# Performance work log

Hardware: AMD Instinct MI355X
Metric: run time of the kernel (lower is better)

Reference implementation:

```python
import jax, jax.numpy as jnp
import numpy as np

N, E, H = 50000, 800000, 64  # nodes, edges, hidden
EPS = 1e-5
SLOPE = 0.2  # LeakyReLU negative slope


def setup_inputs() -> dict:
    key = jax.random.key(0)
    ks = jax.random.split(key, 8)
    return {
        "x": jax.random.normal(ks[0], (N, H), dtype=jnp.float32),
        "edge_weight": jax.random.uniform(ks[1], (E,), dtype=jnp.float32),
        "edge_index": jax.random.randint(ks[2], (2, E), 0, N, dtype=jnp.int64),
        # Linear weights, torch convention [out_features, in_features], bias=False
        "w1": jax.random.normal(ks[3], (H, 2 * H), dtype=jnp.float32) * 0.05,
        "w2": jax.random.normal(ks[4], (H, H), dtype=jnp.float32) * 0.05,
        "w3": jax.random.normal(ks[5], (H, H), dtype=jnp.float32) * 0.05,
        # LayerNorm affine params
        "g1": jnp.ones((2 * H,), jnp.float32), "b1": jnp.zeros((2 * H,), jnp.float32),
        "g2": jnp.ones((H,), jnp.float32), "b2": jnp.zeros((H,), jnp.float32),
        "g3": jnp.ones((H,), jnp.float32), "b3": jnp.zeros((H,), jnp.float32),
    }


def _ln_act_lin(h, g, b, w):
    # LayerNorm -> LeakyReLU(0.2) -> Linear(bias=False), as in MLP(norm='layer')
    mu = jnp.mean(h, axis=-1, keepdims=True)
    var = jnp.mean((h - mu) ** 2, axis=-1, keepdims=True)
    h = (h - mu) * jax.lax.rsqrt(var + EPS) * g + b
    h = jnp.where(h > 0, h, SLOPE * h)
    return h @ w.T


def reference(x, edge_weight, edge_index, w1, w2, w3, g1, b1, g2, b2, g3, b3):
    src, tgt = edge_index[0], edge_index[1]  # x_j = source, x_i = target
    x_j = x[src]                              # [E, H] gather
    x_i = x[tgt]                              # [E, H] gather
    m = jnp.concatenate([x_i, edge_weight[:, None] * (x_j - x_i)], axis=-1)  # [E, 2H]
    m = _ln_act_lin(m, g1, b1, w1)
    m = _ln_act_lin(m, g2, b2, w2)
    m = _ln_act_lin(m, g3, b3, w3)            # [E, H]
    agg = jax.ops.segment_max(m, tgt, num_segments=N)  # EdgeConv aggr='max'
    agg = jnp.where(jnp.isfinite(agg), agg, 0.0)       # isolated nodes -> 0
    return agg + x                             # residual (ResBlock)
```

## Files before the change

### kernel.cpp

```cpp
#include <hip/hip_runtime.h>

#define NN 50000
#define NE 800000
#define NT (NE / 32)

#define CNT_OFF   0u
#define BASE_OFF  204800u
#define PART_OFF  409600u
#define SLOT_OFF  417792u
#define SRCW_OFF  3670016u
#define M_OFF     (1u << 24)
#define WS_NEEDED ((size_t)(1u << 24) + (size_t)NE * 64u * 2u)
#define PB 196

typedef __bf16 bf16x8 __attribute__((ext_vector_type(8)));
typedef float f32x16 __attribute__((ext_vector_type(16)));
typedef unsigned short u16x2 __attribute__((ext_vector_type(2)));

union U4 { unsigned u[4]; __bf16 h[8]; bf16x8 v; };
union PKU { unsigned u; u16x2 v; };

__device__ __forceinline__ unsigned pkpair(float a, float b) {
  union { unsigned u; __bf16 h[2]; } r;
  r.h[0] = (__bf16)a; r.h[1] = (__bf16)b;
  return r.u;
}
__device__ __forceinline__ float bflo(unsigned u) { return __uint_as_float(u << 16); }
__device__ __forceinline__ float bfhi(unsigned u) { return __uint_as_float(u & 0xFFFF0000u); }
__device__ __forceinline__ unsigned pkmaxu16(unsigned a, unsigned b) {
  PKU x, y, r; x.u = a; y.u = b;
  r.v = __builtin_elementwise_max(x.v, y.v);
  return r.u;
}

extern "C" __global__ void __launch_bounds__(256)
scatter_kernel(const int* __restrict__ ei, unsigned* __restrict__ cnt,
               unsigned* __restrict__ slot) {
  const int e = blockIdx.x * 256 + threadIdx.x;
  if (e < NE) {
    int t = ei[NE + e];
    t = min(max(t, 0), NN - 1);
    slot[e] = atomicAdd(cnt + t, 1u);
  }
}

extern "C" __global__ void __launch_bounds__(256)
scan_a_kernel(const unsigned* __restrict__ cnt, unsigned* __restrict__ partial) {
  __shared__ unsigned wsum[4];
  const int t = threadIdx.x, wv = t >> 6, ln = t & 63;
  const int i = blockIdx.x * 256 + t;
  unsigned v = (i < NN) ? cnt[i] : 0u;
  #pragma unroll
  for (int d = 1; d < 64; d <<= 1) v += (unsigned)__shfl_up((int)v, d) * (ln >= d ? 1u : 0u);
  if (ln == 63) wsum[wv] = v;
  __syncthreads();
  if (t == 0) partial[blockIdx.x] = wsum[0] + wsum[1] + wsum[2] + wsum[3];
}

extern "C" __global__ void __launch_bounds__(256)
scan_c_kernel(const unsigned* __restrict__ cnt, const unsigned* __restrict__ partial,
              unsigned* __restrict__ base) {
  __shared__ unsigned pscan[256];
  __shared__ unsigned wsum[4];
  const int t = threadIdx.x, wv = t >> 6, ln = t & 63;
  const unsigned pv = (t < PB) ? partial[t] : 0u;
  unsigned s = pv;
  #pragma unroll
  for (int d = 1; d < 64; d <<= 1) s += (unsigned)__shfl_up((int)s, d) * (ln >= d ? 1u : 0u);
  if (ln == 63) wsum[wv] = s;
  __syncthreads();
  unsigned woff = 0;
  #pragma unroll
  for (int k = 0; k < 4; ++k) woff += (k < wv) ? wsum[k] : 0u;
  pscan[t] = woff + s - pv;
  if (blockIdx.x == 0 && t == 255) base[NN] = woff + s;
  __syncthreads();
  const unsigned blockoff = pscan[blockIdx.x];
  const int i = blockIdx.x * 256 + t;
  const unsigned v = (i < NN) ? cnt[i] : 0u;
  unsigned s2 = v;
  #pragma unroll
  for (int d = 1; d < 64; d <<= 1) s2 += (unsigned)__shfl_up((int)s2, d) * (ln >= d ? 1u : 0u);
  if (ln == 63) wsum[wv] = s2;
  __syncthreads();
  unsigned woff2 = 0;
  #pragma unroll
  for (int k = 0; k < 4; ++k) woff2 += (k < wv) ? wsum[k] : 0u;
  if (i < NN) base[i] = blockoff + woff2 + s2 - v;
}

extern "C" __global__ void __launch_bounds__(256)
reorder_kernel(const int* __restrict__ ei, const float* __restrict__ ew,
               const unsigned* __restrict__ base, const unsigned* __restrict__ slot,
               uint2* __restrict__ srcw) {
  const int e = blockIdx.x * 256 + threadIdx.x;
  if (e < NE) {
    const int s = min(max(ei[e], 0), NN - 1);
    const int t = min(max(ei[NE + e], 0), NN - 1);
    const unsigned pos = base[t] + slot[e];
    uint2 rec;
    rec.x = (unsigned)s | ((unsigned)t << 16);
    rec.y = __float_as_uint(ew[e]);
    srcw[pos] = rec;
  }
}

extern "C" __global__ void __launch_bounds__(256, 3)
edge_mlp_kernel(const float* __restrict__ x, const float* __restrict__ w1,
                const float* __restrict__ w2, const float* __restrict__ w3,
                const float* __restrict__ g1, const float* __restrict__ b1,
                const float* __restrict__ g2, const float* __restrict__ b2,
                const float* __restrict__ g3, const float* __restrict__ b3,
                const uint2* __restrict__ srcw,
                unsigned short* __restrict__ pmax) {
  __shared__ unsigned lds_w[8192];
  const int tid = threadIdx.x;

  #pragma unroll 1
  for (int s = tid; s < 1024; s += 256) {
    const int F = s >> 6, L = s & 63;
    const int t = F >> 1, mt = F & 1;
    const int gg = L >> 5, o = (L & 31) + 32 * mt;
    const float* p = w1 + o * 128 + 16 * t + 8 * gg;
    unsigned* d = &lds_w[(unsigned)(F * 64 + L) * 4u];
    d[0] = pkpair(p[0], p[1]); d[1] = pkpair(p[2], p[3]);
    d[2] = pkpair(p[4], p[5]); d[3] = pkpair(p[6], p[7]);
  }
  #pragma unroll 1
  for (int s = tid; s < 1024; s += 256) {
    const int which = s >> 9, r = s & 511;
    const int F = r >> 6, L = r & 63;
    const int t = F >> 1, mt = F & 1;
    const int gg = L >> 5, o = (L & 31) + 32 * mt;
    const float* W = which ? w3 : w2;
    const float* p = W + o * 64 + 16 * t + 4 * gg;
    unsigned* d = &lds_w[(unsigned)((16 + which * 8 + F) * 64 + L) * 4u];
    d[0] = pkpair(p[0], p[1]); d[1] = pkpair(p[2], p[3]);
    d[2] = pkpair(p[8], p[9]); d[3] = pkpair(p[10], p[11]);
  }
  __syncthreads();

  const int lane = tid & 63;
  const int el = lane & 31;
  const int g = lane >> 5;
  const bf16x8* wfrag = (const bf16x8*)lds_w;

  const int wid = blockIdx.x * 4 + (tid >> 6);
  const int nw = gridDim.x * 4;

  int tile = wid;
  int pvs = 0, pvt = 0; float pw = 0.f;
  if (tile < NT) {
    const uint2 rec = srcw[tile * 32 + el];
    pvs = (int)(rec.x & 0xFFFFu); pvt = (int)(rec.x >> 16); pw = __uint_as_float(rec.y);
  }

  while (tile < NT) {
    asm volatile("" ::: "memory");

    const int p = tile * 32 + el;
    const int vsrc = pvs, vtgt = pvt;
    const float wgt = pw;

    const float* xi = x + (size_t)vtgt * 64 + 8 * g;
    const float* xj = x + (size_t)vsrc * 64 + 8 * g;

    unsigned mp[32];
    float sum = 0.f, ssq = 0.f;
    #pragma unroll
    for (int t = 0; t < 4; ++t) {
      float4 a = *(const float4*)(xi + 16 * t);
      float4 b = *(const float4*)(xi + 16 * t + 4);
      float4 c = *(const float4*)(xj + 16 * t);
      float4 d4 = *(const float4*)(xj + 16 * t + 4);
      float lo[8] = {a.x, a.y, a.z, a.w, b.x, b.y, b.z, b.w};
      float up[8] = {wgt * (c.x - a.x), wgt * (c.y - a.y), wgt * (c.z - a.z), wgt * (c.w - a.w),
                     wgt * (d4.x - b.x), wgt * (d4.y - b.y), wgt * (d4.z - b.z), wgt * (d4.w - b.w)};
      #pragma unroll
      for (int pp = 0; pp < 4; ++pp) {
        mp[4 * t + pp] = pkpair(lo[2 * pp], lo[2 * pp + 1]);
        mp[16 + 4 * t + pp] = pkpair(up[2 * pp], up[2 * pp + 1]);
      }
      #pragma unroll
      for (int j = 0; j < 8; ++j) {
        sum += lo[j] + up[j];
        ssq += lo[j] * lo[j] + up[j] * up[j];
      }
    }

    const int ntile = tile + nw;
    if (ntile < NT) {
      const uint2 rec = srcw[ntile * 32 + el];
      pvs = (int)(rec.x & 0xFFFFu); pvt = (int)(rec.x >> 16); pw = __uint_as_float(rec.y);
    }

    sum += __shfl_xor(sum, 32);
    ssq += __shfl_xor(ssq, 32);
    const float mean1 = sum * (1.f / 128.f);
    const float rstd1 = rsqrtf(ssq * (1.f / 128.f) - mean1 * mean1 + 1e-5f);
    const float c01 = -mean1 * rstd1;

    U4 B1[8];
    #pragma unroll
    for (int t = 0; t < 8; ++t) {
      const int kb = ((t < 4) ? 16 * t : 64 + 16 * (t - 4)) + 8 * g;
      float4 ga = *(const float4*)(g1 + kb);
      float4 gb = *(const float4*)(g1 + kb + 4);
      float4 ba = *(const float4*)(b1 + kb);
      float4 bb = *(const float4*)(b1 + kb + 4);
      float gv[8] = {ga.x, ga.y, ga.z, ga.w, gb.x, gb.y, gb.z, gb.w};
      float bv[8] = {ba.x, ba.y, ba.z, ba.w, bb.x, bb.y, bb.z, bb.w};
      #pragma unroll
      for (int pp = 0; pp < 4; ++pp) {
        const unsigned u = mp[4 * t + pp];
        float v0 = fmaf(bflo(u), rstd1, c01);
        float v1 = fmaf(bfhi(u), rstd1, c01);
        v0 = fmaf(v0, gv[2 * pp], bv[2 * pp]);
        v1 = fmaf(v1, gv[2 * pp + 1], bv[2 * pp + 1]);
        v0 = fmaxf(v0, 0.2f * v0);
        v1 = fmaxf(v1, 0.2f * v1);
        B1[t].h[2 * pp] = (__bf16)v0;
        B1[t].h[2 * pp + 1] = (__bf16)v1;
      }
    }

    f32x16 A0, A1;
    #pragma unroll
    for (int i = 0; i < 16; ++i) { A0[i] = 0.f; A1[i] = 0.f; }
    #pragma unroll
    for (int t = 0; t < 8; ++t) {
      A0 = __builtin_amdgcn_mfma_f32_32x32x16_bf16(wfrag[(2 * t + 0) * 64 + lane], B1[t].v, A0, 0, 0, 0);
      A1 = __builtin_amdgcn_mfma_f32_32x32x16_bf16(wfrag[(2 * t + 1) * 64 + lane], B1[t].v, A1, 0, 0, 0);
    }

    float s2 = 0.f, q2 = 0.f;
    #pragma unroll
    for (int i = 0; i < 16; ++i) {
      s2 += A0[i] + A1[i];
      q2 += A0[i] * A0[i] + A1[i] * A1[i];
    }
    s2 += __shfl_xor(s2, 32); q2 += __shfl_xor(q2, 32);
    const float mean2 = s2 * (1.f / 64.f);
    const float rstd2 = rsqrtf(q2 * (1.f / 64.f) - mean2 * mean2 + 1e-5f);
    const float c02 = -mean2 * rstd2;

    U4 B2[4];
    #pragma unroll
    for (int t2 = 0; t2 < 4; ++t2) {
      const int kb = 16 * t2 + 4 * g;
      float4 gA = *(const float4*)(g2 + kb);
      float4 gB = *(const float4*)(g2 + kb + 8);
      float4 bA = *(const float4*)(b2 + kb);
      float4 bB = *(const float4*)(b2 + kb + 8);
      float gv[8] = {gA.x, gA.y, gA.z, gA.w, gB.x, gB.y, gB.z, gB.w};
      float bv[8] = {bA.x, bA.y, bA.z, bA.w, bB.x, bB.y, bB.z, bB.w};
      #pragma unroll
      for (int j = 0; j < 8; ++j) {
        const int reg = 4 * (2 * (t2 & 1) + (j >> 2)) + (j & 3);
        float v = (t2 >> 1) ? A1[reg] : A0[reg];
        v = fmaf(v, rstd2, c02);
        v = fmaf(v, gv[j], bv[j]);
        v = fmaxf(v, 0.2f * v);
        B2[t2].h[j] = (__bf16)v;
      }
    }

    #pragma unroll
    for (int i = 0; i < 16; ++i) { A0[i] = 0.f; A1[i] = 0.f; }
    #pragma unroll
    for (int t2 = 0; t2 < 4; ++t2) {
      A0 = __builtin_amdgcn_mfma_f32_32x32x16_bf16(wfrag[(16 + 2 * t2 + 0) * 64 + lane], B2[t2].v, A0, 0, 0, 0);
      A1 = __builtin_amdgcn_mfma_f32_32x32x16_bf16(wfrag[(16 + 2 * t2 + 1) * 64 + lane], B2[t2].v, A1, 0, 0, 0);
    }

    float s3 = 0.f, q3 = 0.f;
    #pragma unroll
    for (int i = 0; i < 16; ++i) {
      s3 += A0[i] + A1[i];
      q3 += A0[i] * A0[i] + A1[i] * A1[i];
    }
    s3 += __shfl_xor(s3, 32); q3 += __shfl_xor(q3, 32);
    const float mean3 = s3 * (1.f / 64.f);
    const float rstd3 = rsqrtf(q3 * (1.f / 64.f) - mean3 * mean3 + 1e-5f);
    const float c03 = -mean3 * rstd3;

    U4 B3[4];
    #pragma unroll
    for (int t2 = 0; t2 < 4; ++t2) {
      const int kb = 16 * t2 + 4 * g;
      float4 gA = *(const float4*)(g3 + kb);
      float4 gB = *(const float4*)(g3 + kb + 8);
      float4 bA = *(const float4*)(b3 + kb);
      float4 bB = *(const float4*)(b3 + kb + 8);
      float gv[8] = {gA.x, gA.y, gA.z, gA.w, gB.x, gB.y, gB.z, gB.w};
      float bv[8] = {bA.x, bA.y, bA.z, bA.w, bB.x, bB.y, bB.z, bB.w};
      #pragma unroll
      for (int j = 0; j < 8; ++j) {
        const int reg = 4 * (2 * (t2 & 1) + (j >> 2)) + (j & 3);
        float v = (t2 >> 1) ? A1[reg] : A0[reg];
        v = fmaf(v, rstd3, c03);
        v = fmaf(v, gv[j], bv[j]);
        v = fmaxf(v, 0.2f * v);
        B3[t2].h[j] = (__bf16)v;
      }
    }

    #pragma unroll
    for (int i = 0; i < 16; ++i) { A0[i] = 0.f; A1[i] = 0.f; }
    #pragma unroll
    for (int t2 = 0; t2 < 4; ++t2) {
      A0 = __builtin_amdgcn_mfma_f32_32x32x16_bf16(wfrag[(24 + 2 * t2 + 0) * 64 + lane], B3[t2].v, A0, 0, 0, 0);
      A1 = __builtin_amdgcn_mfma_f32_32x32x16_bf16(wfrag[(24 + 2 * t2 + 1) * 64 + lane], B3[t2].v, A1, 0, 0, 0);
    }

    unsigned P[16];
    #pragma unroll
    for (int q = 0; q < 4; ++q) {
      P[2 * q + 0] = pkpair(A0[4 * q + 0], A0[4 * q + 1]);
      P[2 * q + 1] = pkpair(A0[4 * q + 2], A0[4 * q + 3]);
      P[8 + 2 * q + 0] = pkpair(A1[4 * q + 0], A1[4 * q + 1]);
      P[8 + 2 * q + 1] = pkpair(A1[4 * q + 2], A1[4 * q + 3]);
    }
    #pragma unroll
    for (int i = 0; i < 16; ++i) {
      const unsigned u = P[i];
      const unsigned tt = (u >> 15) & 0x00010001u;
      P[i] = u ^ ((tt << 15) - tt + 0x80008000u);
    }
    #pragma unroll
    for (int d = 1; d < 32; d <<= 1) {
      const int ot = __shfl_down(vtgt, d, 32);
      const bool mrg = (ot == vtgt);
      #pragma unroll
      for (int i = 0; i < 16; ++i) {
        const unsigned pv = __shfl_down(P[i], d, 32);
        const unsigned mx = pkmaxu16(P[i], pv);
        P[i] = mrg ? mx : P[i];
      }
    }
    const int pt = __shfl_up(vtgt, 1, 32);
    if (el == 0 || pt != vtgt) {
      unsigned short* row = pmax + (size_t)p * 64;
      #pragma unroll
      for (int q = 0; q < 4; ++q) {
        uint2 lo; lo.x = P[2 * q]; lo.y = P[2 * q + 1];
        uint2 hi; hi.x = P[8 + 2 * q]; hi.y = P[8 + 2 * q + 1];
        *(uint2*)(row + 8 * q + 4 * g) = lo;
        *(uint2*)(row + 32 + 8 * q + 4 * g) = hi;
      }
    }

    tile = ntile;
  }
}

extern "C" __global__ void __launch_bounds__(256)
gather_max_kernel(const float* __restrict__ x, const unsigned short* __restrict__ pmax,
                  const unsigned* __restrict__ base, float* __restrict__ out) {
  const int node = blockIdx.x * 4 + (threadIdx.x >> 6);
  const int lane = threadIdx.x & 63;
  if (node >= NN) return;

  const unsigned b0 = base[node];
  const unsigned b1 = base[node + 1];
  float maxv = 0.f;
  if (b1 > b0) {
    unsigned kmax = pmax[(size_t)b0 * 64 + lane];
    const unsigned k1 = (b1 - 1) >> 5;
    for (unsigned k = (b0 >> 5) + 1; k <= k1; ++k) {
      kmax = max(kmax, (unsigned)pmax[((size_t)k << 5) * 64 + lane]);
    }
    const unsigned orig = (kmax & 0x8000u) ? (kmax ^ 0x8000u) : (~kmax & 0xFFFFu);
    maxv = __uint_as_float(orig << 16);
  }
  const size_t o = (size_t)node * 64 + lane;
  out[o] = maxv + x[o];
}

extern "C" void kernel_launch(void* const* d_in, const int* in_sizes, int n_in,
                              void* d_out, int out_size, void* d_ws, size_t ws_size,
                              hipStream_t stream) {
  (void)in_sizes; (void)n_in; (void)out_size; (void)ws_size;
  const float* x  = (const float*)d_in[0];
  const float* ew = (const float*)d_in[1];
  const int*   ei = (const int*)d_in[2];
  const float* w1 = (const float*)d_in[3];
  const float* w2 = (const float*)d_in[4];
  const float* w3 = (const float*)d_in[5];
  const float* g1 = (const float*)d_in[6];
  const float* b1 = (const float*)d_in[7];
  const float* g2 = (const float*)d_in[8];
  const float* b2 = (const float*)d_in[9];
  const float* g3 = (const float*)d_in[10];
  const float* b3 = (const float*)d_in[11];

  unsigned* cnt  = (unsigned*)((char*)d_ws + CNT_OFF);
  unsigned* base = (unsigned*)((char*)d_ws + BASE_OFF);
  unsigned* part = (unsigned*)((char*)d_ws + PART_OFF);
  unsigned* slot = (unsigned*)((char*)d_ws + SLOT_OFF);
  uint2*    srcw = (uint2*)((char*)d_ws + SRCW_OFF);
  unsigned short* pmax = (unsigned short*)((char*)d_ws + M_OFF);

  hipMemsetAsync(cnt, 0, (size_t)NN * sizeof(unsigned), stream);
  scatter_kernel<<<(NE + 255) / 256, 256, 0, stream>>>(ei, cnt, slot);
  scan_a_kernel<<<PB, 256, 0, stream>>>(cnt, part);
  scan_c_kernel<<<PB, 256, 0, stream>>>(cnt, part, base);
  reorder_kernel<<<(NE + 255) / 256, 256, 0, stream>>>(ei, ew, base, slot, srcw);
  edge_mlp_kernel<<<3125, 256, 0, stream>>>(x, w1, w2, w3,
                                            g1, b1, g2, b2, g3, b3,
                                            srcw, pmax);
  gather_max_kernel<<<(NN + 3) / 4, 256, 0, stream>>>(x, pmax, base, (float*)d_out);
}
```

Before: 277.3 us.

## Fuse all pipeline stages into one cooperative persistent kernel with grid syncs

Replaces the memset and six separate kernel launches (count, two scan passes, reorder, edge MLP, gather-max) with a single cooperative kernel that separates phases with grid-wide barriers. Weights are staged into LDS once per block at kernel start and reused across all phases. It removes per-launch overhead and inter-kernel gaps, at the cost of grid.sync barriers and of running every phase with the occupancy-limited persistent grid size. The old multi-kernel path is kept as a fallback if the cooperative launch fails.

```diff
diff --git a/kernel.cpp b/kernel.cpp
--- a/kernel.cpp
+++ b/kernel.cpp
@@ -1,4 +1,7 @@
 #include <hip/hip_runtime.h>
+#include <hip/hip_cooperative_groups.h>
+
+namespace cg = cooperative_groups;
 
 #define NN 50000
 #define NE 800000
@@ -10,7 +13,6 @@
 #define SLOT_OFF  417792u
 #define SRCW_OFF  3670016u
 #define M_OFF     (1u << 24)
-#define WS_NEEDED ((size_t)(1u << 24) + (size_t)NE * 64u * 2u)
 #define PB 196
 
 typedef __bf16 bf16x8 __attribute__((ext_vector_type(8)));
@@ -32,6 +34,364 @@
   r.v = __builtin_elementwise_max(x.v, y.v);
   return r.u;
 }
+
+
+__device__ __forceinline__ void stage_weights(const float* __restrict__ w1,
+                                              const float* __restrict__ w2,
+                                              const float* __restrict__ w3,
+                                              unsigned* lds_w, int tid, int bsz) {
+  for (int s = tid; s < 1024; s += bsz) {
+    const int F = s >> 6, L = s & 63;
+    const int t = F >> 1, mt = F & 1;
+    const int gg = L >> 5, o = (L & 31) + 32 * mt;
+    const float* p = w1 + o * 128 + 16 * t + 8 * gg;
+    unsigned* d = &lds_w[(unsigned)(F * 64 + L) * 4u];
+    d[0] = pkpair(p[0], p[1]); d[1] = pkpair(p[2], p[3]);
+    d[2] = pkpair(p[4], p[5]); d[3] = pkpair(p[6], p[7]);
+  }
+  for (int s = tid; s < 1024; s += bsz) {
+    const int which = s >> 9, r = s & 511;
+    const int F = r >> 6, L = r & 63;
+    const int t = F >> 1, mt = F & 1;
+    const int gg = L >> 5, o = (L & 31) + 32 * mt;
+    const float* W = which ? w3 : w2;
+    const float* p = W + o * 64 + 16 * t + 4 * gg;
+    unsigned* d = &lds_w[(unsigned)((16 + which * 8 + F) * 64 + L) * 4u];
+    d[0] = pkpair(p[0], p[1]); d[1] = pkpair(p[2], p[3]);
+    d[2] = pkpair(p[8], p[9]); d[3] = pkpair(p[10], p[11]);
+  }
+}
+
+__device__ __forceinline__ void mlp_tile(
+    const float* __restrict__ x,
+    const float* __restrict__ g1, const float* __restrict__ b1,
+    const float* __restrict__ g2, const float* __restrict__ b2,
+    const float* __restrict__ g3, const float* __restrict__ b3,
+    const bf16x8* wfrag, unsigned short* __restrict__ pmax,
+    int p, int vsrc, int vtgt, float wgt, int lane, int el, int g) {
+  const float* xi = x + (size_t)vtgt * 64 + 8 * g;
+  const float* xj = x + (size_t)vsrc * 64 + 8 * g;
+
+  unsigned mp[32];
+  float sum = 0.f, ssq = 0.f;
+  #pragma unroll
+  for (int t = 0; t < 4; ++t) {
+    float4 a = *(const float4*)(xi + 16 * t);
+    float4 b = *(const float4*)(xi + 16 * t + 4);
+    float4 c = *(const float4*)(xj + 16 * t);
+    float4 d4 = *(const float4*)(xj + 16 * t + 4);
+    float lo[8] = {a.x, a.y, a.z, a.w, b.x, b.y, b.z, b.w};
+    float up[8] = {wgt * (c.x - a.x), wgt * (c.y - a.y), wgt * (c.z - a.z), wgt * (c.w - a.w),
+                   wgt * (d4.x - b.x), wgt * (d4.y - b.y), wgt * (d4.z - b.z), wgt * (d4.w - b.w)};
+    #pragma unroll
+    for (int pp = 0; pp < 4; ++pp) {
+      mp[4 * t + pp] = pkpair(lo[2 * pp], lo[2 * pp + 1]);
+      mp[16 + 4 * t + pp] = pkpair(up[2 * pp], up[2 * pp + 1]);
+    }
+    #pragma unroll
+    for (int j = 0; j < 8; ++j) {
+      sum += lo[j] + up[j];
+      ssq += lo[j] * lo[j] + up[j] * up[j];
+    }
+  }
+
+  sum += __shfl_xor(sum, 32);
+  ssq += __shfl_xor(ssq, 32);
+  const float mean1 = sum * (1.f / 128.f);
+  const float rstd1 = rsqrtf(ssq * (1.f / 128.f) - mean1 * mean1 + 1e-5f);
+  const float c01 = -mean1 * rstd1;
+
+  U4 B1[8];
+  #pragma unroll
+  for (int t = 0; t < 8; ++t) {
+    const int kb = ((t < 4) ? 16 * t : 64 + 16 * (t - 4)) + 8 * g;
+    float4 ga = *(const float4*)(g1 + kb);
+    float4 gb = *(const float4*)(g1 + kb + 4);
+    float4 ba = *(const float4*)(b1 + kb);
+    float4 bb = *(const float4*)(b1 + kb + 4);
+    float gv[8] = {ga.x, ga.y, ga.z, ga.w, gb.x, gb.y, gb.z, gb.w};
+    float bv[8] = {ba.x, ba.y, ba.z, ba.w, bb.x, bb.y, bb.z, bb.w};
+    #pragma unroll
+    for (int pp = 0; pp < 4; ++pp) {
+      const unsigned u = mp[4 * t + pp];
+      float v0 = fmaf(bflo(u), rstd1, c01);
+      float v1 = fmaf(bfhi(u), rstd1, c01);
+      v0 = fmaf(v0, gv[2 * pp], bv[2 * pp]);
+      v1 = fmaf(v1, gv[2 * pp + 1], bv[2 * pp + 1]);
+      v0 = fmaxf(v0, 0.2f * v0);
+      v1 = fmaxf(v1, 0.2f * v1);
+      B1[t].h[2 * pp] = (__bf16)v0;
+      B1[t].h[2 * pp + 1] = (__bf16)v1;
+    }
+  }
+
+  f32x16 A0, A1;
+  #pragma unroll
+  for (int i = 0; i < 16; ++i) { A0[i] = 0.f; A1[i] = 0.f; }
+  #pragma unroll
+  for (int t = 0; t < 8; ++t) {
+    A0 = __builtin_amdgcn_mfma_f32_32x32x16_bf16(wfrag[(2 * t + 0) * 64 + lane], B1[t].v, A0, 0, 0, 0);
+    A1 = __builtin_amdgcn_mfma_f32_32x32x16_bf16(wfrag[(2 * t + 1) * 64 + lane], B1[t].v, A1, 0, 0, 0);
+  }
+
+  float s2 = 0.f, q2 = 0.f;
+  #pragma unroll
+  for (int i = 0; i < 16; ++i) {
+    s2 += A0[i] + A1[i];
+    q2 += A0[i] * A0[i] + A1[i] * A1[i];
+  }
+  s2 += __shfl_xor(s2, 32); q2 += __shfl_xor(q2, 32);
+  const float mean2 = s2 * (1.f / 64.f);
+  const float rstd2 = rsqrtf(q2 * (1.f / 64.f) - mean2 * mean2 + 1e-5f);
+  const float c02 = -mean2 * rstd2;
+
+  U4 B2[4];
+  #pragma unroll
+  for (int t2 = 0; t2 < 4; ++t2) {
+    const int kb = 16 * t2 + 4 * g;
+    float4 gA = *(const float4*)(g2 + kb);
+    float4 gB = *(const float4*)(g2 + kb + 8);
+    float4 bA = *(const float4*)(b2 + kb);
+    float4 bB = *(const float4*)(b2 + kb + 8);
+    float gv[8] = {gA.x, gA.y, gA.z, gA.w, gB.x, gB.y, gB.z, gB.w};
+    float bv[8] = {bA.x, bA.y, bA.z, bA.w, bB.x, bB.y, bB.z, bB.w};
+    #pragma unroll
+    for (int j = 0; j < 8; ++j) {
+      const int reg = 4 * (2 * (t2 & 1) + (j >> 2)) + (j & 3);
+      float v = (t2 >> 1) ? A1[reg] : A0[reg];
+      v = fmaf(v, rstd2, c02);
+      v = fmaf(v, gv[j], bv[j]);
+      v = fmaxf(v, 0.2f * v);
+      B2[t2].h[j] = (__bf16)v;
+    }
+  }
+
+  #pragma unroll
+  for (int i = 0; i < 16; ++i) { A0[i] = 0.f; A1[i] = 0.f; }
+  #pragma unroll
+  for (int t2 = 0; t2 < 4; ++t2) {
+    A0 = __builtin_amdgcn_mfma_f32_32x32x16_bf16(wfrag[(16 + 2 * t2 + 0) * 64 + lane], B2[t2].v, A0, 0, 0, 0);
+    A1 = __builtin_amdgcn_mfma_f32_32x32x16_bf16(wfrag[(16 + 2 * t2 + 1) * 64 + lane], B2[t2].v, A1, 0, 0, 0);
+  }
+
+  float s3 = 0.f, q3 = 0.f;
+  #pragma unroll
+  for (int i = 0; i < 16; ++i) {
+    s3 += A0[i] + A1[i];
+    q3 += A0[i] * A0[i] + A1[i] * A1[i];
+  }
+  s3 += __shfl_xor(s3, 32); q3 += __shfl_xor(q3, 32);
+  const float mean3 = s3 * (1.f / 64.f);
+  const float rstd3 = rsqrtf(q3 * (1.f / 64.f) - mean3 * mean3 + 1e-5f);
+  const float c03 = -mean3 * rstd3;
+
+  U4 B3[4];
+  #pragma unroll
+  for (int t2 = 0; t2 < 4; ++t2) {
+    const int kb = 16 * t2 + 4 * g;
+    float4 gA = *(const float4*)(g3 + kb);
+    float4 gB = *(const float4*)(g3 + kb + 8);
+    float4 bA = *(const float4*)(b3 + kb);
+    float4 bB = *(const float4*)(b3 + kb + 8);
+    float gv[8] = {gA.x, gA.y, gA.z, gA.w, gB.x, gB.y, gB.z, gB.w};
+    float bv[8] = {bA.x, bA.y, bA.z, bA.w, bB.x, bB.y, bB.z, bB.w};
+    #pragma unroll
+    for (int j = 0; j < 8; ++j) {
+      const int reg = 4 * (2 * (t2 & 1) + (j >> 2)) + (j & 3);
+      float v = (t2 >> 1) ? A1[reg] : A0[reg];
+      v = fmaf(v, rstd3, c03);
+      v = fmaf(v, gv[j], bv[j]);
+      v = fmaxf(v, 0.2f * v);
+      B3[t2].h[j] = (__bf16)v;
+    }
+  }
+
+  #pragma unroll
+  for (int i = 0; i < 16; ++i) { A0[i] = 0.f; A1[i] = 0.f; }
+  #pragma unroll
+  for (int t2 = 0; t2 < 4; ++t2) {
+    A0 = __builtin_amdgcn_mfma_f32_32x32x16_bf16(wfrag[(24 + 2 * t2 + 0) * 64 + lane], B3[t2].v, A0, 0, 0, 0);
+    A1 = __builtin_amdgcn_mfma_f32_32x32x16_bf16(wfrag[(24 + 2 * t2 + 1) * 64 + lane], B3[t2].v, A1, 0, 0, 0);
+  }
+
+  unsigned P[16];
+  #pragma unroll
+  for (int q = 0; q < 4; ++q) {
+    P[2 * q + 0] = pkpair(A0[4 * q + 0], A0[4 * q + 1]);
+    P[2 * q + 1] = pkpair(A0[4 * q + 2], A0[4 * q + 3]);
+    P[8 + 2 * q + 0] = pkpair(A1[4 * q + 0], A1[4 * q + 1]);
+    P[8 + 2 * q + 1] = pkpair(A1[4 * q + 2], A1[4 * q + 3]);
+  }
+  #pragma unroll
+  for (int i = 0; i < 16; ++i) {
+    const unsigned u = P[i];
+    const unsigned tt = (u >> 15) & 0x00010001u;
+    P[i] = u ^ ((tt << 15) - tt + 0x80008000u);
+  }
+  int vt = vtgt;
+  #pragma unroll
+  for (int d = 1; d < 32; d <<= 1) {
+    const int ot = __shfl_down(vt, d, 32);
+    const bool mrg = (ot == vt);
+    #pragma unroll
+    for (int i = 0; i < 16; ++i) {
+      const unsigned pv = __shfl_down(P[i], d, 32);
+      const unsigned mx = pkmaxu16(P[i], pv);
+      P[i] = mrg ? mx : P[i];
+    }
+  }
+  const int pt = __shfl_up(vt, 1, 32);
+  if (el == 0 || pt != vt) {
+    unsigned short* row = pmax + (size_t)p * 64;
+    #pragma unroll
+    for (int q = 0; q < 4; ++q) {
+      uint2 lo; lo.x = P[2 * q]; lo.y = P[2 * q + 1];
+      uint2 hi; hi.x = P[8 + 2 * q]; hi.y = P[8 + 2 * q + 1];
+      *(uint2*)(row + 8 * q + 4 * g) = lo;
+      *(uint2*)(row + 32 + 8 * q + 4 * g) = hi;
+    }
+  }
+}
+
+
+extern "C" __global__ void __launch_bounds__(256, 3)
+mega_kernel(const float* __restrict__ x, const float* __restrict__ ew,
+            const int* __restrict__ ei, const float* __restrict__ w1,
+            const float* __restrict__ w2, const float* __restrict__ w3,
+            const float* __restrict__ g1, const float* __restrict__ b1,
+            const float* __restrict__ g2, const float* __restrict__ b2,
+            const float* __restrict__ g3, const float* __restrict__ b3,
+            unsigned* __restrict__ cnt, unsigned* __restrict__ partial,
+            unsigned* __restrict__ base, unsigned* __restrict__ slot,
+            uint2* __restrict__ srcw, unsigned short* __restrict__ pmax,
+            float* __restrict__ out) {
+  cg::grid_group grid = cg::this_grid();
+  __shared__ unsigned lds_w[8192];
+  __shared__ unsigned pscan[256];
+  __shared__ unsigned wsum[4];
+
+  const int tid = threadIdx.x;
+  const int nblk = gridDim.x;
+  const int gthread = blockIdx.x * 256 + tid;
+  const int nthreads = nblk * 256;
+
+  stage_weights(w1, w2, w3, lds_w, tid, 256);
+
+  for (int i = gthread; i < NN; i += nthreads) cnt[i] = 0u;
+  grid.sync();
+
+  for (int e = gthread; e < NE; e += nthreads) {
+    int t = ei[NE + e];
+    t = min(max(t, 0), NN - 1);
+    slot[e] = atomicAdd(cnt + t, 1u);
+  }
+  grid.sync();
+
+  if (blockIdx.x < PB) {
+    const int wv = tid >> 6, ln = tid & 63;
+    const int i = blockIdx.x * 256 + tid;
+    unsigned v = (i < NN) ? cnt[i] : 0u;
+    #pragma unroll
+    for (int d = 1; d < 64; d <<= 1) v += (unsigned)__shfl_up((int)v, d) * (ln >= d ? 1u : 0u);
+    if (ln == 63) wsum[wv] = v;
+    __syncthreads();
+    if (tid == 0) partial[blockIdx.x] = wsum[0] + wsum[1] + wsum[2] + wsum[3];
+  }
+  grid.sync();
+
+  if (blockIdx.x < PB) {
+    const int wv = tid >> 6, ln = tid & 63;
+    const unsigned pv = (tid < PB) ? partial[tid] : 0u;
+    unsigned s = pv;
+    #pragma unroll
+    for (int d = 1; d < 64; d <<= 1) s += (unsigned)__shfl_up((int)s, d) * (ln >= d ? 1u : 0u);
+    if (ln == 63) wsum[wv] = s;
+    __syncthreads();
+    unsigned woff = 0;
+    #pragma unroll
+    for (int k = 0; k < 4; ++k) woff += (k < wv) ? wsum[k] : 0u;
+    pscan[tid] = woff + s - pv;
+    if (blockIdx.x == 0 && tid == 255) base[NN] = woff + s;
+    __syncthreads();
+    const unsigned blockoff = pscan[blockIdx.x];
+    const int i = blockIdx.x * 256 + tid;
+    const unsigned v = (i < NN) ? cnt[i] : 0u;
+    unsigned s2 = v;
+    #pragma unroll
+    for (int d = 1; d < 64; d <<= 1) s2 += (unsigned)__shfl_up((int)s2, d) * (ln >= d ? 1u : 0u);
+    if (ln == 63) wsum[wv] = s2;
+    __syncthreads();
+    unsigned woff2 = 0;
+    #pragma unroll
+    for (int k = 0; k < 4; ++k) woff2 += (k < wv) ? wsum[k] : 0u;
+    if (i < NN) base[i] = blockoff + woff2 + s2 - v;
+  }
+  grid.sync();
+
+  for (int e = gthread; e < NE; e += nthreads) {
+    const int s = min(max(ei[e], 0), NN - 1);
+    const int t = min(max(ei[NE + e], 0), NN - 1);
+    const unsigned pos = base[t] + slot[e];
+    uint2 rec;
+    rec.x = (unsigned)s | ((unsigned)t << 16);
+    rec.y = __float_as_uint(ew[e]);
+    srcw[pos] = rec;
+  }
+  grid.sync();
+
+  {
+    const int lane = tid & 63;
+    const int el = lane & 31;
+    const int g = lane >> 5;
+    const bf16x8* wfrag = (const bf16x8*)lds_w;
+    const int wid = blockIdx.x * 4 + (tid >> 6);
+    const int nw = nblk * 4;
+
+    int tile = wid;
+    int pvs = 0, pvt = 0; float pw = 0.f;
+    if (tile < NT) {
+      const uint2 rec = srcw[tile * 32 + el];
+      pvs = (int)(rec.x & 0xFFFFu); pvt = (int)(rec.x >> 16); pw = __uint_as_float(rec.y);
+    }
+    while (tile < NT) {
+      asm volatile("" ::: "memory");
+      const int p = tile * 32 + el;
+      const int vsrc = pvs, vtgt = pvt;
+      const float wgt = pw;
+      const int ntile = tile + nw;
+      if (ntile < NT) {
+        const uint2 rec = srcw[ntile * 32 + el];
+        pvs = (int)(rec.x & 0xFFFFu); pvt = (int)(rec.x >> 16); pw = __uint_as_float(rec.y);
+      }
+      mlp_tile(x, g1, b1, g2, b2, g3, b3, wfrag, pmax, p, vsrc, vtgt, wgt, lane, el, g);
+      tile = ntile;
+    }
+  }
+  grid.sync();
+
+  {
+    const int lane = tid & 63;
+    const int gwave = blockIdx.x * 4 + (tid >> 6);
+    const int nwave = nblk * 4;
+    for (int node = gwave; node < NN; node += nwave) {
+      const unsigned b0 = base[node];
+      const unsigned b1v = base[node + 1];
+      float maxv = 0.f;
+      if (b1v > b0) {
+        unsigned kmax = pmax[(size_t)b0 * 64 + lane];
+        const unsigned k1 = (b1v - 1) >> 5;
+        for (unsigned k = (b0 >> 5) + 1; k <= k1; ++k) {
+          kmax = max(kmax, (unsigned)pmax[((size_t)k << 5) * 64 + lane]);
+        }
+        const unsigned orig = (kmax & 0x8000u) ? (kmax ^ 0x8000u) : (~kmax & 0xFFFFu);
+        maxv = __uint_as_float(orig << 16);
+      }
+      const size_t o = (size_t)node * 64 + lane;
+      out[o] = maxv + x[o];
+    }
+  }
+}
+
 
 extern "C" __global__ void __launch_bounds__(256)
 scatter_kernel(const int* __restrict__ ei, unsigned* __restrict__ cnt,
@@ -115,36 +475,13 @@
                 unsigned short* __restrict__ pmax) {
   __shared__ unsigned lds_w[8192];
   const int tid = threadIdx.x;
-
-  #pragma unroll 1
-  for (int s = tid; s < 1024; s += 256) {
-    const int F = s >> 6, L = s & 63;
-    const int t = F >> 1, mt = F & 1;
-    const int gg = L >> 5, o = (L & 31) + 32 * mt;
-    const float* p = w1 + o * 128 + 16 * t + 8 * gg;
-    unsigned* d = &lds_w[(unsigned)(F * 64 + L) * 4u];
-    d[0] = pkpair(p[0], p[1]); d[1] = pkpair(p[2], p[3]);
-    d[2] = pkpair(p[4], p[5]); d[3] = pkpair(p[6], p[7]);
-  }
-  #pragma unroll 1
-  for (int s = tid; s < 1024; s += 256) {
-    const int which = s >> 9, r = s & 511;
-    const int F = r >> 6, L = r & 63;
-    const int t = F >> 1, mt = F & 1;
-    const int gg = L >> 5, o = (L & 31) + 32 * mt;
-    const float* W = which ? w3 : w2;
-    const float* p = W + o * 64 + 16 * t + 4 * gg;
-    unsigned* d = &lds_w[(unsigned)((16 + which * 8 + F) * 64 + L) * 4u];
-    d[0] = pkpair(p[0], p[1]); d[1] = pkpair(p[2], p[3]);
-    d[2] = pkpair(p[8], p[9]); d[3] = pkpair(p[10], p[11]);
-  }
+  stage_weights(w1, w2, w3, lds_w, tid, 256);
   __syncthreads();
 
   const int lane = tid & 63;
   const int el = lane & 31;
   const int g = lane >> 5;
   const bf16x8* wfrag = (const bf16x8*)lds_w;
-
   const int wid = blockIdx.x * 4 + (tid >> 6);
   const int nw = gridDim.x * 4;
 
@@ -154,202 +491,17 @@
     const uint2 rec = srcw[tile * 32 + el];
     pvs = (int)(rec.x & 0xFFFFu); pvt = (int)(rec.x >> 16); pw = __uint_as_float(rec.y);
   }
-
   while (tile < NT) {
     asm volatile("" ::: "memory");
-
     const int p = tile * 32 + el;
     const int vsrc = pvs, vtgt = pvt;
     const float wgt = pw;
-
-    const float* xi = x + (size_t)vtgt * 64 + 8 * g;
-    const float* xj = x + (size_t)vsrc * 64 + 8 * g;
-
-    unsigned mp[32];
-    float sum = 0.f, ssq = 0.f;
-    #pragma unroll
-    for (int t = 0; t < 4; ++t) {
-      float4 a = *(const float4*)(xi + 16 * t);
-      float4 b = *(const float4*)(xi + 16 * t + 4);
-      float4 c = *(const float4*)(xj + 16 * t);
-      float4 d4 = *(const float4*)(xj + 16 * t + 4);
-      float lo[8] = {a.x, a.y, a.z, a.w, b.x, b.y, b.z, b.w};
-      float up[8] = {wgt * (c.x - a.x), wgt * (c.y - a.y), wgt * (c.z - a.z), wgt * (c.w - a.w),
-                     wgt * (d4.x - b.x), wgt * (d4.y - b.y), wgt * (d4.z - b.z), wgt * (d4.w - b.w)};
-      #pragma unroll
-      for (int pp = 0; pp < 4; ++pp) {
-        mp[4 * t + pp] = pkpair(lo[2 * pp], lo[2 * pp + 1]);
-        mp[16 + 4 * t + pp] = pkpair(up[2 * pp], up[2 * pp + 1]);
-      }
-      #pragma unroll
-      for (int j = 0; j < 8; ++j) {
-        sum += lo[j] + up[j];
-        ssq += lo[j] * lo[j] + up[j] * up[j];
-      }
-    }
-
     const int ntile = tile + nw;
     if (ntile < NT) {
       const uint2 rec = srcw[ntile * 32 + el];
       pvs = (int)(rec.x & 0xFFFFu); pvt = (int)(rec.x >> 16); pw = __uint_as_float(rec.y);
     }
-
-    sum += __shfl_xor(sum, 32);
-    ssq += __shfl_xor(ssq, 32);
-    const float mean1 = sum * (1.f / 128.f);
-    const float rstd1 = rsqrtf(ssq * (1.f / 128.f) - mean1 * mean1 + 1e-5f);
-    const float c01 = -mean1 * rstd1;
-
-    U4 B1[8];
-    #pragma unroll
-    for (int t = 0; t < 8; ++t) {
-      const int kb = ((t < 4) ? 16 * t : 64 + 16 * (t - 4)) + 8 * g;
-      float4 ga = *(const float4*)(g1 + kb);
-      float4 gb = *(const float4*)(g1 + kb + 4);
-      float4 ba = *(const float4*)(b1 + kb);
-      float4 bb = *(const float4*)(b1 + kb + 4);
-      float gv[8] = {ga.x, ga.y, ga.z, ga.w, gb.x, gb.y, gb.z, gb.w};
-      float bv[8] = {ba.x, ba.y, ba.z, ba.w, bb.x, bb.y, bb.z, bb.w};
-      #pragma unroll
-      for (int pp = 0; pp < 4; ++pp) {
-        const unsigned u = mp[4 * t + pp];
-        float v0 = fmaf(bflo(u), rstd1, c01);
-        float v1 = fmaf(bfhi(u), rstd1, c01);
-        v0 = fmaf(v0, gv[2 * pp], bv[2 * pp]);
-        v1 = fmaf(v1, gv[2 * pp + 1], bv[2 * pp + 1]);
-        v0 = fmaxf(v0, 0.2f * v0);
-        v1 = fmaxf(v1, 0.2f * v1);
-        B1[t].h[2 * pp] = (__bf16)v0;
-        B1[t].h[2 * pp + 1] = (__bf16)v1;
-      }
-    }
-
-    f32x16 A0, A1;
-    #pragma unroll
-    for (int i = 0; i < 16; ++i) { A0[i] = 0.f; A1[i] = 0.f; }
-    #pragma unroll
-    for (int t = 0; t < 8; ++t) {
-      A0 = __builtin_amdgcn_mfma_f32_32x32x16_bf16(wfrag[(2 * t + 0) * 64 + lane], B1[t].v, A0, 0, 0, 0);
-      A1 = __builtin_amdgcn_mfma_f32_32x32x16_bf16(wfrag[(2 * t + 1) * 64 + lane], B1[t].v, A1, 0, 0, 0);
-    }
-
-    float s2 = 0.f, q2 = 0.f;
-    #pragma unroll
-    for (int i = 0; i < 16; ++i) {
-      s2 += A0[i] + A1[i];
-      q2 += A0[i] * A0[i] + A1[i] * A1[i];
-    }
-    s2 += __shfl_xor(s2, 32); q2 += __shfl_xor(q2, 32);
-    const float mean2 = s2 * (1.f / 64.f);
-    const float rstd2 = rsqrtf(q2 * (1.f / 64.f) - mean2 * mean2 + 1e-5f);
-    const float c02 = -mean2 * rstd2;
-
-    U4 B2[4];
-    #pragma unroll
-    for (int t2 = 0; t2 < 4; ++t2) {
-      const int kb = 16 * t2 + 4 * g;
-      float4 gA = *(const float4*)(g2 + kb);
-      float4 gB = *(const float4*)(g2 + kb + 8);
-      float4 bA = *(const float4*)(b2 + kb);
-      float4 bB = *(const float4*)(b2 + kb + 8);
-      float gv[8] = {gA.x, gA.y, gA.z, gA.w, gB.x, gB.y, gB.z, gB.w};
-      float bv[8] = {bA.x, bA.y, bA.z, bA.w, bB.x, bB.y, bB.z, bB.w};
-      #pragma unroll
-      for (int j = 0; j < 8; ++j) {
-        const int reg = 4 * (2 * (t2 & 1) + (j >> 2)) + (j & 3);
-        float v = (t2 >> 1) ? A1[reg] : A0[reg];
-        v = fmaf(v, rstd2, c02);
-        v = fmaf(v, gv[j], bv[j]);
-        v = fmaxf(v, 0.2f * v);
-        B2[t2].h[j] = (__bf16)v;
-      }
-    }
-
-    #pragma unroll
-    for (int i = 0; i < 16; ++i) { A0[i] = 0.f; A1[i] = 0.f; }
-    #pragma unroll
-    for (int t2 = 0; t2 < 4; ++t2) {
-      A0 = __builtin_amdgcn_mfma_f32_32x32x16_bf16(wfrag[(16 + 2 * t2 + 0) * 64 + lane], B2[t2].v, A0, 0, 0, 0);
-      A1 = __builtin_amdgcn_mfma_f32_32x32x16_bf16(wfrag[(16 + 2 * t2 + 1) * 64 + lane], B2[t2].v, A1, 0, 0, 0);
-    }
-
-    float s3 = 0.f, q3 = 0.f;
-    #pragma unroll
-    for (int i = 0; i < 16; ++i) {
-      s3 += A0[i] + A1[i];
-      q3 += A0[i] * A0[i] + A1[i] * A1[i];
-    }
-    s3 += __shfl_xor(s3, 32); q3 += __shfl_xor(q3, 32);
-    const float mean3 = s3 * (1.f / 64.f);
-    const float rstd3 = rsqrtf(q3 * (1.f / 64.f) - mean3 * mean3 + 1e-5f);
-    const float c03 = -mean3 * rstd3;
-
-    U4 B3[4];
-    #pragma unroll
-    for (int t2 = 0; t2 < 4; ++t2) {
-      const int kb = 16 * t2 + 4 * g;
-      float4 gA = *(const float4*)(g3 + kb);
-      float4 gB = *(const float4*)(g3 + kb + 8);
-      float4 bA = *(const float4*)(b3 + kb);
-      float4 bB = *(const float4*)(b3 + kb + 8);
-      float gv[8] = {gA.x, gA.y, gA.z, gA.w, gB.x, gB.y, gB.z, gB.w};
-      float bv[8] = {bA.x, bA.y, bA.z, bA.w, bB.x, bB.y, bB.z, bB.w};
-      #pragma unroll
-      for (int j = 0; j < 8; ++j) {
-        const int reg = 4 * (2 * (t2 & 1) + (j >> 2)) + (j & 3);
-        float v = (t2 >> 1) ? A1[reg] : A0[reg];
-        v = fmaf(v, rstd3, c03);
-        v = fmaf(v, gv[j], bv[j]);
-        v = fmaxf(v, 0.2f * v);
-        B3[t2].h[j] = (__bf16)v;
-      }
-    }
-
-    #pragma unroll
-    for (int i = 0; i < 16; ++i) { A0[i] = 0.f; A1[i] = 0.f; }
-    #pragma unroll
-    for (int t2 = 0; t2 < 4; ++t2) {
-      A0 = __builtin_amdgcn_mfma_f32_32x32x16_bf16(wfrag[(24 + 2 * t2 + 0) * 64 + lane], B3[t2].v, A0, 0, 0, 0);
-      A1 = __builtin_amdgcn_mfma_f32_32x32x16_bf16(wfrag[(24 + 2 * t2 + 1) * 64 + lane], B3[t2].v, A1, 0, 0, 0);
-    }
-
-    unsigned P[16];
-    #pragma unroll
-    for (int q = 0; q < 4; ++q) {
-      P[2 * q + 0] = pkpair(A0[4 * q + 0], A0[4 * q + 1]);
-      P[2 * q + 1] = pkpair(A0[4 * q + 2], A0[4 * q + 3]);
-      P[8 + 2 * q + 0] = pkpair(A1[4 * q + 0], A1[4 * q + 1]);
-      P[8 + 2 * q + 1] = pkpair(A1[4 * q + 2], A1[4 * q + 3]);
-    }
-    #pragma unroll
-    for (int i = 0; i < 16; ++i) {
-      const unsigned u = P[i];
-      const unsigned tt = (u >> 15) & 0x00010001u;
-      P[i] = u ^ ((tt << 15) - tt + 0x80008000u);
-    }
-    #pragma unroll
-    for (int d = 1; d < 32; d <<= 1) {
-      const int ot = __shfl_down(vtgt, d, 32);
-      const bool mrg = (ot == vtgt);
-      #pragma unroll
-      for (int i = 0; i < 16; ++i) {
-        const unsigned pv = __shfl_down(P[i], d, 32);
-        const unsigned mx = pkmaxu16(P[i], pv);
-        P[i] = mrg ? mx : P[i];
-      }
-    }
-    const int pt = __shfl_up(vtgt, 1, 32);
-    if (el == 0 || pt != vtgt) {
-      unsigned short* row = pmax + (size_t)p * 64;
-      #pragma unroll
-      for (int q = 0; q < 4; ++q) {
-        uint2 lo; lo.x = P[2 * q]; lo.y = P[2 * q + 1];
-        uint2 hi; hi.x = P[8 + 2 * q]; hi.y = P[8 + 2 * q + 1];
-        *(uint2*)(row + 8 * q + 4 * g) = lo;
-        *(uint2*)(row + 32 + 8 * q + 4 * g) = hi;
-      }
-    }
-
+    mlp_tile(x, g1, b1, g2, b2, g3, b3, wfrag, pmax, p, vsrc, vtgt, wgt, lane, el, g);
     tile = ntile;
   }
 }
@@ -360,13 +512,12 @@
   const int node = blockIdx.x * 4 + (threadIdx.x >> 6);
   const int lane = threadIdx.x & 63;
   if (node >= NN) return;
-
   const unsigned b0 = base[node];
-  const unsigned b1 = base[node + 1];
+  const unsigned b1v = base[node + 1];
   float maxv = 0.f;
-  if (b1 > b0) {
+  if (b1v > b0) {
     unsigned kmax = pmax[(size_t)b0 * 64 + lane];
-    const unsigned k1 = (b1 - 1) >> 5;
+    const unsigned k1 = (b1v - 1) >> 5;
     for (unsigned k = (b0 >> 5) + 1; k <= k1; ++k) {
       kmax = max(kmax, (unsigned)pmax[((size_t)k << 5) * 64 + lane]);
     }
@@ -376,6 +527,7 @@
   const size_t o = (size_t)node * 64 + lane;
   out[o] = maxv + x[o];
 }
+
 
 extern "C" void kernel_launch(void* const* d_in, const int* in_sizes, int n_in,
                               void* d_out, int out_size, void* d_ws, size_t ws_size,
@@ -400,14 +552,33 @@
   unsigned* slot = (unsigned*)((char*)d_ws + SLOT_OFF);
   uint2*    srcw = (uint2*)((char*)d_ws + SRCW_OFF);
   unsigned short* pmax = (unsigned short*)((char*)d_ws + M_OFF);
-
-  hipMemsetAsync(cnt, 0, (size_t)NN * sizeof(unsigned), stream);
-  scatter_kernel<<<(NE + 255) / 256, 256, 0, stream>>>(ei, cnt, slot);
-  scan_a_kernel<<<PB, 256, 0, stream>>>(cnt, part);
-  scan_c_kernel<<<PB, 256, 0, stream>>>(cnt, part, base);
-  reorder_kernel<<<(NE + 255) / 256, 256, 0, stream>>>(ei, ew, base, slot, srcw);
-  edge_mlp_kernel<<<3125, 256, 0, stream>>>(x, w1, w2, w3,
-                                            g1, b1, g2, b2, g3, b3,
-                                            srcw, pmax);
-  gather_max_kernel<<<(NN + 3) / 4, 256, 0, stream>>>(x, pmax, base, (float*)d_out);
-}
+  float* out = (float*)d_out;
+
+  int blocksPerCU = 0;
+  hipError_t qerr = hipOccupancyMaxActiveBlocksPerMultiprocessor(
+      &blocksPerCU, (const void*)mega_kernel, 256, 0);
+  int nblk = (qerr == hipSuccess) ? blocksPerCU * 256 : 0;
+
+  hipError_t lerr = hipErrorUnknown;
+  if (nblk >= 256) {
+    void* args[] = {
+      (void*)&x, (void*)&ew, (void*)&ei, (void*)&w1, (void*)&w2, (void*)&w3,
+      (void*)&g1, (void*)&b1, (void*)&g2, (void*)&b2, (void*)&g3, (void*)&b3,
+      (void*)&cnt, (void*)&part, (void*)&base, (void*)&slot,
+      (void*)&srcw, (void*)&pmax, (void*)&out
+    };
+    lerr = hipLaunchCooperativeKernel((void*)mega_kernel, dim3(nblk), dim3(256),
+                                      args, 0, stream);
+  }
+
+  if (lerr != hipSuccess) {
+    hipMemsetAsync(cnt, 0, (size_t)NN * sizeof(unsigned), stream);
+    scatter_kernel<<<(NE + 255) / 256, 256, 0, stream>>>(ei, cnt, slot);
+    scan_a_kernel<<<PB, 256, 0, stream>>>(cnt, part);
+    scan_c_kernel<<<PB, 256, 0, stream>>>(cnt, part, base);
+    reorder_kernel<<<(NE + 255) / 256, 256, 0, stream>>>(ei, ew, base, slot, srcw);
+    edge_mlp_kernel<<<3125, 256, 0, stream>>>(x, w1, w2, w3,
+                                              g1, b1, g2, b2, g3, b3, srcw, pmax);
+    gather_max_kernel<<<(NN + 3) / 4, 256, 0, stream>>>(x, pmax, base, out);
+  }
+}
```

Result: slower. 502.8 us (+81.3%).
